# Optimization experiments

Measured on AMD Instinct MI355X. Metric: run time of the kernel, lower is better.

Reference implementation:

```python
import jax, jax.numpy as jnp
import numpy as np

D, H, L, V, BS = 1024, 16, 12, 50257, 2048
HD = D // H
EPS = 1e-5


def _ln(x, w, b):
    m = jnp.mean(x, -1, keepdims=True)
    v = jnp.mean(jnp.square(x - m), -1, keepdims=True)
    return (x - m) * jax.lax.rsqrt(v + EPS) * w + b


def setup_inputs() -> dict:
    key = jax.random.key(0)
    ks = jax.random.split(key, 10)
    B, T = 4, 1024
    s = 0.02
    return {
        "idx": jax.random.randint(ks[0], (B, T), 0, V),
        "targets": jax.random.randint(ks[1], (B, T), 0, V),
        "wte": s * jax.random.normal(ks[2], (V, D), jnp.float32),
        "wpe": s * jax.random.normal(ks[3], (BS, D), jnp.float32),
        "ln1_w": jnp.ones((L, D), jnp.float32),
        "ln1_b": jnp.zeros((L, D), jnp.float32),
        "qkv_w": s * jax.random.normal(ks[4], (L, D, 3 * D), jnp.float32),
        "qkv_b": jnp.zeros((L, 3 * D), jnp.float32),
        "o_w": s * jax.random.normal(ks[5], (L, D, D), jnp.float32),
        "o_b": jnp.zeros((L, D), jnp.float32),
        "ln2_w": jnp.ones((L, D), jnp.float32),
        "ln2_b": jnp.zeros((L, D), jnp.float32),
        "up_w": s * jax.random.normal(ks[6], (L, D, 4 * D), jnp.float32),
        "up_b": jnp.zeros((L, 4 * D), jnp.float32),
        "down_w": s * jax.random.normal(ks[7], (L, 4 * D, D), jnp.float32),
        "down_b": jnp.zeros((L, D), jnp.float32),
        "lnf_w": jnp.ones((D,), jnp.float32),
        "lnf_b": jnp.zeros((D,), jnp.float32),
        "lm_b": jnp.zeros((V,), jnp.float32),
    }


def _gpt(idx, targets, wte, wpe, ln1_w, ln1_b, qkv_w, qkv_b, o_w, o_b,
         ln2_w, ln2_b, up_w, up_b, down_w, down_b, lnf_w, lnf_b, lm_b):
    B, T = idx.shape
    x = wte[idx] + wpe[:T][None, :, :]  # [B,T,D]
    causal = jnp.tril(jnp.ones((T, T), bool))
    scale = HD ** -0.5

    def block(h, p):
        (l1w, l1b, qw, qb, ow, ob, l2w, l2b, uw, ub, dw, db) = p
        y = _ln(h, l1w, l1b)
        qkv = y @ qw + qb  # [B,T,3D]
        q, k, v = jnp.split(qkv, 3, axis=-1)
        q = q.reshape(B, T, H, HD)
        k = k.reshape(B, T, H, HD)
        v = v.reshape(B, T, H, HD)
        scores = jnp.einsum('bqhd,bkhd->bhqk', q, k) * scale
        scores = jnp.where(causal, scores, -jnp.inf)
        attn = jax.nn.softmax(scores, axis=-1)
        o = jnp.einsum('bhqk,bkhd->bqhd', attn, v).reshape(B, T, D)
        h = h + o @ ow + ob
        y = _ln(h, l2w, l2b)
        y = jax.nn.gelu(y @ uw + ub, approximate=False)
        h = h + y @ dw + db
        return h, None

    params = (ln1_w, ln1_b, qkv_w, qkv_b, o_w, o_b, ln2_w, ln2_b, up_w, up_b, down_w, down_b)
    x, _ = jax.lax.scan(block, x, params)
    x = _ln(x, lnf_w, lnf_b)
    logits = x @ wte.T + lm_b  # tied lm_head weight
    logp = jax.nn.log_softmax(logits, axis=-1)
    nll = -jnp.take_along_axis(logp, targets[..., None], axis=-1)[..., 0]
    loss = jnp.mean(nll)
    return logits, loss


def reference(idx, targets, wte, wpe, ln1_w, ln1_b, qkv_w, qkv_b, o_w, o_b,
              ln2_w, ln2_b, up_w, up_b, down_w, down_b, lnf_w, lnf_b, lm_b):
    return _gpt(idx, targets, wte, wpe, ln1_w, ln1_b, qkv_w, qkv_b, o_w, o_b,
                ln2_w, ln2_b, up_w, up_b, down_w, down_b, lnf_w, lnf_b, lm_b)
```

## Files before the change

kernel.cpp:

```cpp
#include <hip/hip_runtime.h>
#include <hip/hip_bf16.h>
#include <math.h>

typedef __attribute__((ext_vector_type(8))) short bfrag;
typedef __attribute__((ext_vector_type(4))) float f32x4;

static constexpr int Dm = 1024, Hh = 16, HD = 64, Ll = 12, Tt = 1024, Bb = 4;
static constexpr int Vv = 50257, Mrows = 4096;

__device__ inline unsigned short f2bf(float f) {
    unsigned u = __float_as_uint(f);
    u += 0x7fffu + ((u >> 16) & 1u);
    return (unsigned short)(u >> 16);
}
__device__ inline float bf2f(unsigned short s) {
    return __uint_as_float(((unsigned)s) << 16);
}

__device__ inline void gload16(const unsigned short* g, unsigned short* l) {
    __builtin_amdgcn_global_load_lds(
        (const __attribute__((address_space(1))) void*)g,
        (__attribute__((address_space(3))) void*)l, 16, 0, 0);
}

__global__ __launch_bounds__(256)
void embed_kernel(float* __restrict__ x, const float* __restrict__ wte,
                  const float* __restrict__ wpe, const int* __restrict__ idx) {
    int row = blockIdx.x;
    int t = row & (Tt - 1);
    int id = idx[row];
    int c = threadIdx.x * 4;
    float4 a = *reinterpret_cast<const float4*>(&wte[(size_t)id * Dm + c]);
    float4 p = *reinterpret_cast<const float4*>(&wpe[(size_t)t * Dm + c]);
    float4 o;
    o.x = a.x + p.x; o.y = a.y + p.y; o.z = a.z + p.z; o.w = a.w + p.w;
    *reinterpret_cast<float4*>(&x[(size_t)row * Dm + c]) = o;
}

__global__ __launch_bounds__(256)
void ln_kernel(unsigned short* __restrict__ y, const float* __restrict__ x,
               const float* __restrict__ w, const float* __restrict__ b) {
    int row = blockIdx.x;
    int tid = threadIdx.x;
    int lane = tid & 63, wv = tid >> 6;
    const float* xr = x + (size_t)row * Dm;
    float4 v = *reinterpret_cast<const float4*>(&xr[tid * 4]);
    float s1 = v.x + v.y + v.z + v.w;
    float s2 = v.x * v.x + v.y * v.y + v.z * v.z + v.w * v.w;
#pragma unroll
    for (int off = 1; off < 64; off <<= 1) {
        s1 += __shfl_xor(s1, off);
        s2 += __shfl_xor(s2, off);
    }
    __shared__ float r1[4], r2[4];
    if (lane == 0) { r1[wv] = s1; r2[wv] = s2; }
    __syncthreads();
    s1 = r1[0] + r1[1] + r1[2] + r1[3];
    s2 = r2[0] + r2[1] + r2[2] + r2[3];
    float mean = s1 * (1.0f / Dm);
    float var = s2 * (1.0f / Dm) - mean * mean;
    float rstd = rsqrtf(var + 1e-5f);
    float4 wvv = *reinterpret_cast<const float4*>(&w[tid * 4]);
    float4 bv = *reinterpret_cast<const float4*>(&b[tid * 4]);
    ushort4 o;
    o.x = f2bf((v.x - mean) * rstd * wvv.x + bv.x);
    o.y = f2bf((v.y - mean) * rstd * wvv.y + bv.y);
    o.z = f2bf((v.z - mean) * rstd * wvv.z + bv.z);
    o.w = f2bf((v.w - mean) * rstd * wvv.w + bv.w);
    *reinterpret_cast<ushort4*>(&y[(size_t)row * Dm + tid * 4]) = o;
}

__global__ __launch_bounds__(256)
void transpose_layer(const float* __restrict__ qw, const float* __restrict__ ow,
                     const float* __restrict__ uw, const float* __restrict__ dw,
                     unsigned short* __restrict__ wTq, unsigned short* __restrict__ wTo,
                     unsigned short* __restrict__ wTu, unsigned short* __restrict__ wTd) {
    __shared__ float t[32][33];
    int tb = blockIdx.x;
    const float* src; unsigned short* dst; int K, N, nx, base;
    if (tb < 3072)      { src = qw; dst = wTq; K = 1024; N = 3072; nx = 96;  base = 0; }
    else if (tb < 4096) { src = ow; dst = wTo; K = 1024; N = 1024; nx = 32;  base = 3072; }
    else if (tb < 8192) { src = uw; dst = wTu; K = 1024; N = 4096; nx = 128; base = 4096; }
    else                { src = dw; dst = wTd; K = 4096; N = 1024; nx = 32;  base = 8192; }
    int tt = tb - base;
    int n0 = (tt % nx) * 32, k0 = (tt / nx) * 32;
    int tid = threadIdx.x;
    int r = tid >> 3, c4 = (tid & 7) * 4;
    float4 v = *reinterpret_cast<const float4*>(&src[(size_t)(k0 + r) * N + n0 + c4]);
    t[r][c4] = v.x; t[r][c4 + 1] = v.y; t[r][c4 + 2] = v.z; t[r][c4 + 3] = v.w;
    __syncthreads();
    int nr = tid >> 3, kc = (tid & 7) * 4;
    ushort4 o;
    o.x = f2bf(t[kc][nr]);
    o.y = f2bf(t[kc + 1][nr]);
    o.z = f2bf(t[kc + 2][nr]);
    o.w = f2bf(t[kc + 3][nr]);
    *reinterpret_cast<ushort4*>(&dst[(size_t)(n0 + nr) * K + k0 + kc]) = o;
}

__global__ __launch_bounds__(128)
void cvt_rows(unsigned short* __restrict__ dst, const float* __restrict__ src) {
    int row = blockIdx.x;
    int t = threadIdx.x;
    const float* s = src + (size_t)row * Dm + t * 8;
    float4 f0 = *reinterpret_cast<const float4*>(s);
    float4 f1 = *reinterpret_cast<const float4*>(s + 4);
    ushort4 o0, o1;
    o0.x = f2bf(f0.x); o0.y = f2bf(f0.y); o0.z = f2bf(f0.z); o0.w = f2bf(f0.w);
    o1.x = f2bf(f1.x); o1.y = f2bf(f1.y); o1.z = f2bf(f1.z); o1.w = f2bf(f1.w);
    unsigned short* d = dst + (size_t)row * Dm + t * 8;
    *reinterpret_cast<ushort4*>(d) = o0;
    *reinterpret_cast<ushort4*>(d + 4) = o1;
}

template<int EPI, int GN>
__global__ __launch_bounds__(512, 2)
void gemm256(const unsigned short* __restrict__ A, const unsigned short* __restrict__ B,
             const float* __restrict__ bias, void* __restrict__ Cp,
             int Nv, int K, int ldc, int ncol) {
    __shared__ unsigned short As[4][256 * 32];
    __shared__ unsigned short Bs[4][256 * 32];
    const int tid = threadIdx.x;
    const int lane = tid & 63, w = tid >> 6;
    const int wr = w >> 2, wc = w & 3;
    const int g = lane >> 4, lr = lane & 15;
    const int slotk = (lr >> 1) & 3;

    const int gx = gridDim.x;
    int flat = blockIdx.y * gx + blockIdx.x;
    int nwg = gx * gridDim.y;
    {
        int q = nwg >> 3, rr = nwg & 7;
        int xcd = flat & 7, pos = flat >> 3;
        flat = ((xcd < rr) ? (xcd * (q + 1)) : (rr * (q + 1) + (xcd - rr) * q)) + pos;
    }
    const int bm = (flat % gx) * 256;
    const int bn = (flat / gx) * 256;

    const int srow = lane >> 2;
    const int gsrc = (lane & 3) ^ ((lane >> 3) & 3);
    const int rA0 = (w * 2 + 0) * 16 + srow;
    const int rA1 = (w * 2 + 1) * 16 + srow;
    const size_t aoff0 = (size_t)(bm + rA0) * K + gsrc * 8;
    const size_t aoff1 = (size_t)(bm + rA1) * K + gsrc * 8;
    int gb0 = bn + rA0, gb1 = bn + rA1;
    if (GN) { gb0 = (gb0 < Nv) ? gb0 : (Nv - 1); gb1 = (gb1 < Nv) ? gb1 : (Nv - 1); }
    const size_t boff0 = (size_t)gb0 * K + gsrc * 8;
    const size_t boff1 = (size_t)gb1 * K + gsrc * 8;
    unsigned short* lA0 = &As[0][(w * 2 + 0) * 512];
    unsigned short* lA1 = &As[0][(w * 2 + 1) * 512];
    unsigned short* lB0 = &Bs[0][(w * 2 + 0) * 512];
    unsigned short* lB1 = &Bs[0][(w * 2 + 1) * 512];

    const int nt = K >> 5;

    f32x4 acc[8][4];
#pragma unroll
    for (int i = 0; i < 8; ++i)
#pragma unroll
        for (int j = 0; j < 4; ++j)
#pragma unroll
            for (int r = 0; r < 4; ++r) acc[i][j][r] = 0.f;

#pragma unroll
    for (int tp = 0; tp < 3; ++tp) {
        const int kp = tp << 5;
        gload16(A + aoff0 + kp, lA0 + tp * 8192);
        gload16(B + boff0 + kp, lB0 + tp * 8192);
        gload16(A + aoff1 + kp, lA1 + tp * 8192);
        gload16(B + boff1 + kp, lB1 + tp * 8192);
    }
    asm volatile("s_waitcnt vmcnt(8)" ::: "memory");
    asm volatile("s_barrier" ::: "memory");

    for (int t = 0; t < nt; ++t) {
        const int bt = t & 3;
        const unsigned short* as = As[bt];
        const unsigned short* bs = Bs[bt];
        const int pf = t + 3;
        const int kp = pf << 5;
        const int so = (pf & 3) * 8192;

        bfrag bfr[4], af[8];
#pragma unroll
        for (int ni = 0; ni < 4; ++ni) {
            int row = wc * 64 + ni * 16 + lr;
            bfr[ni] = *reinterpret_cast<const bfrag*>(&bs[row * 32 + ((g ^ slotk) * 8)]);
        }
#pragma unroll
        for (int mi = 0; mi < 8; ++mi) {
            int row = wr * 128 + mi * 16 + lr;
            af[mi] = *reinterpret_cast<const bfrag*>(&as[row * 32 + ((g ^ slotk) * 8)]);
        }
        if (pf < nt) {
            gload16(A + aoff0 + kp, lA0 + so);
            gload16(B + boff0 + kp, lB0 + so);
            gload16(A + aoff1 + kp, lA1 + so);
            gload16(B + boff1 + kp, lB1 + so);
        }
        __builtin_amdgcn_s_setprio(1);
#pragma unroll
        for (int mi = 0; mi < 8; ++mi)
#pragma unroll
            for (int ni = 0; ni < 4; ++ni)
                acc[mi][ni] = __builtin_amdgcn_mfma_f32_16x16x32_bf16(
                    af[mi], bfr[ni], acc[mi][ni], 0, 0, 0);
        __builtin_amdgcn_s_setprio(0);
        if (t + 3 < nt)      asm volatile("s_waitcnt vmcnt(8)" ::: "memory");
        else if (t + 2 < nt) asm volatile("s_waitcnt vmcnt(4)" ::: "memory");
        else if (t + 1 < nt) asm volatile("s_waitcnt vmcnt(0)" ::: "memory");
        asm volatile("s_barrier" ::: "memory");
    }

    unsigned short* Cb = (unsigned short*)Cp;
    float* Cf = (float*)Cp;
#pragma unroll
    for (int ni = 0; ni < 4; ++ni) {
        int col = bn + wc * 64 + ni * 16 + lr;
        if (GN && col >= Nv) continue;
        int gcol = ncol + col;
        float bi = bias[gcol];
#pragma unroll
        for (int mi = 0; mi < 8; ++mi) {
            int row0 = bm + wr * 128 + mi * 16 + g * 4;
#pragma unroll
            for (int r = 0; r < 4; ++r) {
                int row = row0 + r;
                float v = acc[mi][ni][r] + bi;
                if (EPI == 0) {
                    Cb[(size_t)row * ldc + gcol] = f2bf(v);
                } else if (EPI == 1) {
                    v = 0.5f * v * (1.0f + erff(v * 0.70710678118654752f));
                    Cb[(size_t)row * ldc + gcol] = f2bf(v);
                } else {
                    Cf[(size_t)row * ldc + gcol] = v;
                }
            }
        }
    }
}

template<int EPI>
__global__ __launch_bounds__(256, 2)
void gemm128p(const unsigned short* __restrict__ A, const unsigned short* __restrict__ B,
              const float* __restrict__ bias, const float* __restrict__ R,
              void* __restrict__ Cp, int K, int ldc) {
    __shared__ unsigned short As[4][128 * 32];
    __shared__ unsigned short Bs[4][128 * 32];
    const int tid = threadIdx.x;
    const int lane = tid & 63, w = tid >> 6;
    const int wr = w >> 1, wc = w & 1;
    const int g = lane >> 4, lr = lane & 15;
    const int slotk = (lr >> 1) & 3;

    const int gx = gridDim.x;
    int flat = blockIdx.y * gx + blockIdx.x;
    int nwg = gx * gridDim.y;
    {
        int q = nwg >> 3, rr = nwg & 7;
        int xcd = flat & 7, pos = flat >> 3;
        flat = ((xcd < rr) ? (xcd * (q + 1)) : (rr * (q + 1) + (xcd - rr) * q)) + pos;
    }
    const int bm = (flat % gx) * 128;
    const int bn = (flat / gx) * 128;

    const int srow = lane >> 2;
    const int gsrc = (lane & 3) ^ ((lane >> 3) & 3);
    const int rA0 = (w * 2 + 0) * 16 + srow;
    const int rA1 = (w * 2 + 1) * 16 + srow;
    const size_t aoff0 = (size_t)(bm + rA0) * K + gsrc * 8;
    const size_t aoff1 = (size_t)(bm + rA1) * K + gsrc * 8;
    const size_t boff0 = (size_t)(bn + rA0) * K + gsrc * 8;
    const size_t boff1 = (size_t)(bn + rA1) * K + gsrc * 8;
    unsigned short* lA0 = &As[0][(w * 2 + 0) * 512];
    unsigned short* lA1 = &As[0][(w * 2 + 1) * 512];
    unsigned short* lB0 = &Bs[0][(w * 2 + 0) * 512];
    unsigned short* lB1 = &Bs[0][(w * 2 + 1) * 512];

    const int nt = K >> 5;

    f32x4 acc[4][4];
#pragma unroll
    for (int i = 0; i < 4; ++i)
#pragma unroll
        for (int j = 0; j < 4; ++j)
#pragma unroll
            for (int r = 0; r < 4; ++r) acc[i][j][r] = 0.f;

#pragma unroll
    for (int tp = 0; tp < 3; ++tp) {
        const int kp = tp << 5;
        gload16(A + aoff0 + kp, lA0 + tp * 4096);
        gload16(B + boff0 + kp, lB0 + tp * 4096);
        gload16(A + aoff1 + kp, lA1 + tp * 4096);
        gload16(B + boff1 + kp, lB1 + tp * 4096);
    }
    asm volatile("s_waitcnt vmcnt(8)" ::: "memory");
    asm volatile("s_barrier" ::: "memory");

    for (int t = 0; t < nt; ++t) {
        const int bt = t & 3;
        const unsigned short* as = As[bt];
        const unsigned short* bs = Bs[bt];
        const int pf = t + 3;
        const int kp = pf << 5;
        const int so = (pf & 3) * 4096;

        bfrag af[4], bfr[4];
#pragma unroll
        for (int i = 0; i < 4; ++i) {
            int ra = wr * 64 + i * 16 + lr;
            af[i] = *reinterpret_cast<const bfrag*>(&as[ra * 32 + ((g ^ slotk) * 8)]);
            int rb = wc * 64 + i * 16 + lr;
            bfr[i] = *reinterpret_cast<const bfrag*>(&bs[rb * 32 + ((g ^ slotk) * 8)]);
        }
        if (pf < nt) {
            gload16(A + aoff0 + kp, lA0 + so);
            gload16(B + boff0 + kp, lB0 + so);
            gload16(A + aoff1 + kp, lA1 + so);
            gload16(B + boff1 + kp, lB1 + so);
        }
        __builtin_amdgcn_s_setprio(1);
#pragma unroll
        for (int mi = 0; mi < 4; ++mi)
#pragma unroll
            for (int ni = 0; ni < 4; ++ni)
                acc[mi][ni] = __builtin_amdgcn_mfma_f32_16x16x32_bf16(
                    af[mi], bfr[ni], acc[mi][ni], 0, 0, 0);
        __builtin_amdgcn_s_setprio(0);
        if (t + 3 < nt)      asm volatile("s_waitcnt vmcnt(8)" ::: "memory");
        else if (t + 2 < nt) asm volatile("s_waitcnt vmcnt(4)" ::: "memory");
        else if (t + 1 < nt) asm volatile("s_waitcnt vmcnt(0)" ::: "memory");
        asm volatile("s_barrier" ::: "memory");
    }

    unsigned short* Cb = (unsigned short*)Cp;
    float* Cf = (float*)Cp;
#pragma unroll
    for (int ni = 0; ni < 4; ++ni) {
        int col = bn + wc * 64 + ni * 16 + lr;
        float bi = bias[col];
#pragma unroll
        for (int mi = 0; mi < 4; ++mi) {
            int row0 = bm + wr * 64 + mi * 16 + g * 4;
#pragma unroll
            for (int r = 0; r < 4; ++r) {
                int row = row0 + r;
                float v = acc[mi][ni][r] + bi;
                if (EPI == 0) {
                    Cb[(size_t)row * ldc + col] = f2bf(v);
                } else {
                    Cf[(size_t)row * ldc + col] = R[(size_t)row * ldc + col] + v;
                }
            }
        }
    }
}

__global__ __launch_bounds__(256)
void attn_mfma(const unsigned short* __restrict__ qkv, unsigned short* __restrict__ ob) {
    const int bq = blockIdx.x;
    const int h = blockIdx.y;
    const int b = blockIdx.z;
    const int tid = threadIdx.x, lane = tid & 63, w = tid >> 6;
    const int g = lane >> 4, lr = lane & 15;
    const int qg0 = bq * 128 + w * 32;

    __shared__ unsigned short Kt[64 * 72];
    __shared__ unsigned short Vt[64 * 72];
    __shared__ unsigned short Pl[4][32 * 72];
    unsigned short* Plw = Pl[w];

    bfrag aq[2][2];
#pragma unroll
    for (int qs = 0; qs < 2; ++qs)
#pragma unroll
        for (int ks = 0; ks < 2; ++ks) {
            int row = qg0 + qs * 16 + lr;
            aq[qs][ks] = *reinterpret_cast<const bfrag*>(
                &qkv[(size_t)(b * Tt + row) * 3072 + h * 64 + ks * 32 + g * 8]);
        }

    float mrow[2][4], lrow[2][4], osc[2][4];
    f32x4 oacc[2][4];
#pragma unroll
    for (int qs = 0; qs < 2; ++qs)
#pragma unroll
        for (int r = 0; r < 4; ++r) { mrow[qs][r] = -3.0e38f; lrow[qs][r] = 0.f; }
#pragma unroll
    for (int qs = 0; qs < 2; ++qs)
#pragma unroll
        for (int dn = 0; dn < 4; ++dn)
#pragma unroll
            for (int r = 0; r < 4; ++r) oacc[qs][dn][r] = 0.f;

    const int ntile = 2 * bq + 2;
    for (int kt = 0; kt < ntile; ++kt) {
        {
            int row = tid >> 2, seg = tid & 3;
            const unsigned short* sk =
                &qkv[(size_t)(b * Tt + kt * 64 + row) * 3072 + Dm + h * 64 + seg * 16];
            bfrag kv0 = *(const bfrag*)sk;
            bfrag kv1 = *(const bfrag*)(sk + 8);
            *reinterpret_cast<bfrag*>(&Kt[row * 72 + seg * 16]) = kv0;
            *reinterpret_cast<bfrag*>(&Kt[row * 72 + seg * 16 + 8]) = kv1;
            const uint4* sv = reinterpret_cast<const uint4*>(
                &qkv[(size_t)(b * Tt + kt * 64 + row) * 3072 + 2 * Dm + h * 64 + seg * 16]);
            uint4 u0 = sv[0], u1 = sv[1];
            uint4 a, r0, r1;
            a.x = (seg & 1) ? u0.y : u0.x; a.y = (seg & 1) ? u0.z : u0.y;
            a.z = (seg & 1) ? u0.w : u0.z; a.w = (seg & 1) ? u0.x : u0.w;
            r0.x = (seg & 2) ? a.z : a.x; r0.y = (seg & 2) ? a.w : a.y;
            r0.z = (seg & 2) ? a.x : a.z; r0.w = (seg & 2) ? a.y : a.w;
            a.x = (seg & 1) ? u1.y : u1.x; a.y = (seg & 1) ? u1.z : u1.y;
            a.z = (seg & 1) ? u1.w : u1.z; a.w = (seg & 1) ? u1.x : u1.w;
            r1.x = (seg & 2) ? a.z : a.x; r1.y = (seg & 2) ? a.w : a.y;
            r1.z = (seg & 2) ? a.x : a.z; r1.w = (seg & 2) ? a.y : a.w;
            unsigned w0[4] = {r0.x, r0.y, r0.z, r0.w};
            unsigned w1[4] = {r1.x, r1.y, r1.z, r1.w};
#pragma unroll
            for (int i = 0; i < 8; ++i) {
                int j = (i + 2 * seg) & 7;
                unsigned ww = w0[i >> 1];
                unsigned short val = (i & 1) ? (unsigned short)(ww >> 16)
                                             : (unsigned short)(ww & 0xffff);
                Vt[(seg * 16 + j) * 72 + row] = val;
            }
#pragma unroll
            for (int i = 0; i < 8; ++i) {
                int j = (i + 2 * seg) & 7;
                unsigned ww = w1[i >> 1];
                unsigned short val = (i & 1) ? (unsigned short)(ww >> 16)
                                             : (unsigned short)(ww & 0xffff);
                Vt[(seg * 16 + 8 + j) * 72 + row] = val;
            }
        }
        __syncthreads();

        bool active = (kt * 64 <= qg0 + 31);
        if (active) {
            f32x4 s[2][4];
#pragma unroll
            for (int qs = 0; qs < 2; ++qs)
#pragma unroll
                for (int n = 0; n < 4; ++n)
#pragma unroll
                    for (int r = 0; r < 4; ++r) s[qs][n][r] = 0.f;
            bfrag bk[4][2];
#pragma unroll
            for (int n = 0; n < 4; ++n)
#pragma unroll
                for (int ks = 0; ks < 2; ++ks)
                    bk[n][ks] = *reinterpret_cast<const bfrag*>(
                        &Kt[(n * 16 + lr) * 72 + ks * 32 + g * 8]);
#pragma unroll
            for (int qs = 0; qs < 2; ++qs)
#pragma unroll
                for (int n = 0; n < 4; ++n)
#pragma unroll
                    for (int ks = 0; ks < 2; ++ks)
                        s[qs][n] = __builtin_amdgcn_mfma_f32_16x16x32_bf16(
                            aq[qs][ks], bk[n][ks], s[qs][n], 0, 0, 0);

            bool mayMask = (kt * 64 + 63 > qg0);
            float pv[2][4][4];
#pragma unroll
            for (int qs = 0; qs < 2; ++qs) {
#pragma unroll
                for (int r = 0; r < 4; ++r) {
                    int qrow = qg0 + qs * 16 + g * 4 + r;
                    float v[4];
#pragma unroll
                    for (int n = 0; n < 4; ++n) {
                        float sv = s[qs][n][r] * 0.125f;
                        if (mayMask && (kt * 64 + n * 16 + lr > qrow)) sv = -3.0e38f;
                        v[n] = sv;
                    }
                    float tmax = fmaxf(fmaxf(v[0], v[1]), fmaxf(v[2], v[3]));
                    tmax = fmaxf(tmax, __shfl_xor(tmax, 1));
                    tmax = fmaxf(tmax, __shfl_xor(tmax, 2));
                    tmax = fmaxf(tmax, __shfl_xor(tmax, 4));
                    tmax = fmaxf(tmax, __shfl_xor(tmax, 8));
                    float mold = mrow[qs][r];
                    float mnew = fmaxf(mold, tmax);
                    float scl = expf(mold - mnew);
                    float psum = 0.f;
#pragma unroll
                    for (int n = 0; n < 4; ++n) {
                        float p = expf(v[n] - mnew);
                        pv[qs][n][r] = p;
                        psum += p;
                    }
                    psum += __shfl_xor(psum, 1);
                    psum += __shfl_xor(psum, 2);
                    psum += __shfl_xor(psum, 4);
                    psum += __shfl_xor(psum, 8);
                    lrow[qs][r] = lrow[qs][r] * scl + psum;
                    mrow[qs][r] = mnew;
                    osc[qs][r] = scl;
                }
            }
#pragma unroll
            for (int qs = 0; qs < 2; ++qs)
#pragma unroll
                for (int dn = 0; dn < 4; ++dn)
#pragma unroll
                    for (int r = 0; r < 4; ++r) oacc[qs][dn][r] *= osc[qs][r];
#pragma unroll
            for (int qs = 0; qs < 2; ++qs)
#pragma unroll
                for (int n = 0; n < 4; ++n)
#pragma unroll
                    for (int r = 0; r < 4; ++r)
                        Plw[(qs * 16 + g * 4 + r) * 72 + n * 16 + lr] = f2bf(pv[qs][n][r]);
            asm volatile("s_waitcnt lgkmcnt(0)" ::: "memory");
            bfrag ap[2][2], bv[4][2];
#pragma unroll
            for (int qs = 0; qs < 2; ++qs)
#pragma unroll
                for (int ks = 0; ks < 2; ++ks)
                    ap[qs][ks] = *reinterpret_cast<const bfrag*>(
                        &Plw[(qs * 16 + lr) * 72 + ks * 32 + g * 8]);
#pragma unroll
            for (int dn = 0; dn < 4; ++dn)
#pragma unroll
                for (int ks = 0; ks < 2; ++ks)
                    bv[dn][ks] = *reinterpret_cast<const bfrag*>(
                        &Vt[(dn * 16 + lr) * 72 + ks * 32 + g * 8]);
#pragma unroll
            for (int qs = 0; qs < 2; ++qs)
#pragma unroll
                for (int dn = 0; dn < 4; ++dn)
#pragma unroll
                    for (int ks = 0; ks < 2; ++ks)
                        oacc[qs][dn] = __builtin_amdgcn_mfma_f32_16x16x32_bf16(
                            ap[qs][ks], bv[dn][ks], oacc[qs][dn], 0, 0, 0);
        }
        __syncthreads();
    }

#pragma unroll
    for (int qs = 0; qs < 2; ++qs)
#pragma unroll
        for (int r = 0; r < 4; ++r) {
            float rinv = 1.0f / lrow[qs][r];
            int qrow = qg0 + qs * 16 + g * 4 + r;
#pragma unroll
            for (int dn = 0; dn < 4; ++dn)
                ob[(size_t)(b * Tt + qrow) * Dm + h * 64 + dn * 16 + lr] =
                    f2bf(oacc[qs][dn][r] * rinv);
        }
}

__global__ __launch_bounds__(512)
void loss_row_kernel(float* __restrict__ nll, const float* __restrict__ logits,
                     const int* __restrict__ targets) {
    const int row = blockIdx.x;
    const int tid = threadIdx.x;
    const int lane = tid & 63, wv = tid >> 6;
    const float* lr = logits + (size_t)row * Vv;

    const int lead = (4 - (row & 3)) & 3;
    const int nvec = (Vv - lead) >> 2;
    const int tail = Vv - lead - (nvec << 2);

    float m = -3.0e38f, s = 0.f;
    if (tid < lead) {
        float v = lr[tid];
        m = v; s = 1.f;
    }
    for (int k = tid; k < nvec; k += 512) {
        float4 v = *reinterpret_cast<const float4*>(lr + lead + (k << 2));
        float tm = fmaxf(fmaxf(v.x, v.y), fmaxf(v.z, v.w));
        float nm = fmaxf(m, tm);
        s = s * __expf(m - nm)
          + __expf(v.x - nm) + __expf(v.y - nm) + __expf(v.z - nm) + __expf(v.w - nm);
        m = nm;
    }
    if (tid < tail) {
        float v = lr[lead + (nvec << 2) + tid];
        float nm = fmaxf(m, v);
        s = s * __expf(m - nm) + __expf(v - nm);
        m = nm;
    }
#pragma unroll
    for (int off = 1; off < 64; off <<= 1) {
        float om = __shfl_xor(m, off);
        float os = __shfl_xor(s, off);
        float nm = fmaxf(m, om);
        s = s * __expf(m - nm) + os * __expf(om - nm);
        m = nm;
    }
    __shared__ float rm[8], rs[8];
    if (lane == 0) { rm[wv] = m; rs[wv] = s; }
    __syncthreads();
    if (tid == 0) {
        float M = rm[0];
#pragma unroll
        for (int i = 1; i < 8; ++i) M = fmaxf(M, rm[i]);
        float S = 0.f;
#pragma unroll
        for (int i = 0; i < 8; ++i) S += rs[i] * __expf(rm[i] - M);
        float lse = M + __logf(S);
        nll[row] = lse - lr[targets[row]];
    }
}

__global__ __launch_bounds__(256)
void loss_reduce_kernel(float* __restrict__ loss, const float* __restrict__ nll) {
    int tid = threadIdx.x;
    __shared__ float red[256];
    float s = 0.f;
    for (int j = tid; j < Mrows; j += 256) s += nll[j];
    red[tid] = s;
    __syncthreads();
    for (int st = 128; st > 0; st >>= 1) {
        if (tid < st) red[tid] += red[tid + st];
        __syncthreads();
    }
    if (tid == 0) *loss = red[0] * (1.0f / Mrows);
}

extern "C" void kernel_launch(void* const* d_in, const int* in_sizes, int n_in,
                              void* d_out, int out_size, void* d_ws, size_t ws_size,
                              hipStream_t stream) {
    const int* idx = (const int*)d_in[0];
    const int* targets = (const int*)d_in[1];
    const float* wte = (const float*)d_in[2];
    const float* wpe = (const float*)d_in[3];
    const float* ln1_w = (const float*)d_in[4];
    const float* ln1_b = (const float*)d_in[5];
    const float* qkv_w = (const float*)d_in[6];
    const float* qkv_b = (const float*)d_in[7];
    const float* o_w = (const float*)d_in[8];
    const float* o_b = (const float*)d_in[9];
    const float* ln2_w = (const float*)d_in[10];
    const float* ln2_b = (const float*)d_in[11];
    const float* up_w = (const float*)d_in[12];
    const float* up_b = (const float*)d_in[13];
    const float* down_w = (const float*)d_in[14];
    const float* down_b = (const float*)d_in[15];
    const float* lnf_w = (const float*)d_in[16];
    const float* lnf_b = (const float*)d_in[17];
    const float* lm_b = (const float*)d_in[18];

    float* logits = (float*)d_out;
    char* ws = (char*)d_ws;
    const size_t MB = 1 << 20;
    float* x            = (float*)(ws);
    unsigned short* y   = (unsigned short*)(ws + 16 * MB);
    unsigned short* qkv = (unsigned short*)(ws + 24 * MB);
    unsigned short* ob  = (unsigned short*)(ws + 48 * MB);
    unsigned short* up  = (unsigned short*)(ws + 56 * MB);
    unsigned short* wTq = (unsigned short*)(ws + 88 * MB);
    unsigned short* wTo = (unsigned short*)(ws + 96 * MB);
    unsigned short* wTu = (unsigned short*)(ws + 100 * MB);
    unsigned short* wTd = (unsigned short*)(ws + 112 * MB);
    float* nll          = (float*)(ws + 127 * MB);
    unsigned short* wbf = (unsigned short*)(ws + 24 * MB);

    embed_kernel<<<Mrows, 256, 0, stream>>>(x, wte, wpe, idx);

    for (int l = 0; l < Ll; ++l) {
        ln_kernel<<<Mrows, 256, 0, stream>>>(y, x, ln1_w + l * Dm, ln1_b + l * Dm);
        transpose_layer<<<12288, 256, 0, stream>>>(
            qkv_w + (size_t)l * Dm * 3 * Dm, o_w + (size_t)l * Dm * Dm,
            up_w + (size_t)l * Dm * 4 * Dm, down_w + (size_t)l * 4 * Dm * Dm,
            wTq, wTo, wTu, wTd);
        gemm128p<0><<<dim3(Mrows / 128, 3 * Dm / 128), 256, 0, stream>>>(
            y, wTq, qkv_b + (size_t)l * 3 * Dm, nullptr, qkv, Dm, 3 * Dm);
        attn_mfma<<<dim3(8, Hh, Bb), 256, 0, stream>>>(qkv, ob);
        gemm128p<2><<<dim3(Mrows / 128, Dm / 128), 256, 0, stream>>>(
            ob, wTo, o_b + (size_t)l * Dm, x, x, Dm, Dm);
        ln_kernel<<<Mrows, 256, 0, stream>>>(y, x, ln2_w + l * Dm, ln2_b + l * Dm);
        gemm256<1, 0><<<dim3(Mrows / 256, 4 * Dm / 256), 512, 0, stream>>>(
            y, wTu, up_b + (size_t)l * 4 * Dm, up, 4 * Dm, Dm, 4 * Dm, 0);
        gemm128p<2><<<dim3(Mrows / 128, Dm / 128), 256, 0, stream>>>(
            up, wTd, down_b + (size_t)l * Dm, x, x, 4 * Dm, Dm);
    }

    ln_kernel<<<Mrows, 256, 0, stream>>>(y, x, lnf_w, lnf_b);

    cvt_rows<<<Vv, 128, 0, stream>>>(wbf, wte);
    gemm256<3, 1><<<dim3(Mrows / 256, (Vv + 255) / 256), 512, 0, stream>>>(
        y, wbf, lm_b, logits, Vv, Dm, Vv, 0);

    loss_row_kernel<<<Mrows, 512, 0, stream>>>(nll, logits, targets);
    loss_reduce_kernel<<<1, 256, 0, stream>>>(logits + (size_t)Mrows * Vv, nll);
}
```

Measured before the change: 4.622 ms.

## Switch gemm256 to double-buffered BK=64 tiles with nontemporal fp32 stores

Restructures the 256x256 GEMM mainloop from a 4-stage ring of K=32 tiles to a 2-stage double buffer of K=64 tiles. Each thread now loads 16B rows with an 8-way XOR swizzle, and each loaded tile feeds two MFMA sub-steps. This halves the number of barriers and waitcnts per K and lowers occupancy to 1 block per CU, which lets the compiler use more registers. In exchange only one tile is prefetched ahead, so global-load latency is less well hidden. The fp32 epilogue, used for the large logits output, now writes with nontemporal stores to reduce cache pollution.

```diff
diff --git a/kernel.cpp b/kernel.cpp
--- a/kernel.cpp
+++ b/kernel.cpp
@@ -114,17 +114,16 @@
 }
 
 template<int EPI, int GN>
-__global__ __launch_bounds__(512, 2)
+__global__ __launch_bounds__(512, 1)
 void gemm256(const unsigned short* __restrict__ A, const unsigned short* __restrict__ B,
              const float* __restrict__ bias, void* __restrict__ Cp,
              int Nv, int K, int ldc, int ncol) {
-    __shared__ unsigned short As[4][256 * 32];
-    __shared__ unsigned short Bs[4][256 * 32];
+    __shared__ unsigned short As[2][256 * 64];
+    __shared__ unsigned short Bs[2][256 * 64];
     const int tid = threadIdx.x;
     const int lane = tid & 63, w = tid >> 6;
     const int wr = w >> 2, wc = w & 3;
     const int g = lane >> 4, lr = lane & 15;
-    const int slotk = (lr >> 1) & 3;
 
     const int gx = gridDim.x;
     int flat = blockIdx.y * gx + blockIdx.x;
@@ -137,22 +136,19 @@
     const int bm = (flat % gx) * 256;
     const int bn = (flat / gx) * 256;
 
-    const int srow = lane >> 2;
-    const int gsrc = (lane & 3) ^ ((lane >> 3) & 3);
-    const int rA0 = (w * 2 + 0) * 16 + srow;
-    const int rA1 = (w * 2 + 1) * 16 + srow;
-    const size_t aoff0 = (size_t)(bm + rA0) * K + gsrc * 8;
-    const size_t aoff1 = (size_t)(bm + rA1) * K + gsrc * 8;
-    int gb0 = bn + rA0, gb1 = bn + rA1;
-    if (GN) { gb0 = (gb0 < Nv) ? gb0 : (Nv - 1); gb1 = (gb1 < Nv) ? gb1 : (Nv - 1); }
-    const size_t boff0 = (size_t)gb0 * K + gsrc * 8;
-    const size_t boff1 = (size_t)gb1 * K + gsrc * 8;
-    unsigned short* lA0 = &As[0][(w * 2 + 0) * 512];
-    unsigned short* lA1 = &As[0][(w * 2 + 1) * 512];
-    unsigned short* lB0 = &Bs[0][(w * 2 + 0) * 512];
-    unsigned short* lB1 = &Bs[0][(w * 2 + 1) * 512];
-
-    const int nt = K >> 5;
+    const int srow = tid >> 3;
+    const int gsrc = (tid & 7) ^ (srow & 7);
+    size_t aoff[4], boff[4];
+#pragma unroll
+    for (int j = 0; j < 4; ++j) {
+        int ra = bm + j * 64 + srow;
+        aoff[j] = (size_t)ra * K + gsrc * 8;
+        int rb = bn + j * 64 + srow;
+        if (GN) rb = (rb < Nv) ? rb : (Nv - 1);
+        boff[j] = (size_t)rb * K + gsrc * 8;
+    }
+
+    const int nt = K >> 6;
 
     f32x4 acc[8][4];
 #pragma unroll
@@ -163,53 +159,54 @@
             for (int r = 0; r < 4; ++r) acc[i][j][r] = 0.f;
 
 #pragma unroll
-    for (int tp = 0; tp < 3; ++tp) {
-        const int kp = tp << 5;
-        gload16(A + aoff0 + kp, lA0 + tp * 8192);
-        gload16(B + boff0 + kp, lB0 + tp * 8192);
-        gload16(A + aoff1 + kp, lA1 + tp * 8192);
-        gload16(B + boff1 + kp, lB1 + tp * 8192);
-    }
-    asm volatile("s_waitcnt vmcnt(8)" ::: "memory");
+    for (int j = 0; j < 4; ++j) {
+        gload16(A + aoff[j], &As[0][j * 4096 + tid * 8]);
+        gload16(B + boff[j], &Bs[0][j * 4096 + tid * 8]);
+    }
+    asm volatile("s_waitcnt vmcnt(0)" ::: "memory");
     asm volatile("s_barrier" ::: "memory");
 
     for (int t = 0; t < nt; ++t) {
-        const int bt = t & 3;
-        const unsigned short* as = As[bt];
-        const unsigned short* bs = Bs[bt];
-        const int pf = t + 3;
-        const int kp = pf << 5;
-        const int so = (pf & 3) * 8192;
-
-        bfrag bfr[4], af[8];
-#pragma unroll
-        for (int ni = 0; ni < 4; ++ni) {
-            int row = wc * 64 + ni * 16 + lr;
-            bfr[ni] = *reinterpret_cast<const bfrag*>(&bs[row * 32 + ((g ^ slotk) * 8)]);
-        }
-#pragma unroll
-        for (int mi = 0; mi < 8; ++mi) {
-            int row = wr * 128 + mi * 16 + lr;
-            af[mi] = *reinterpret_cast<const bfrag*>(&as[row * 32 + ((g ^ slotk) * 8)]);
-        }
-        if (pf < nt) {
-            gload16(A + aoff0 + kp, lA0 + so);
-            gload16(B + boff0 + kp, lB0 + so);
-            gload16(A + aoff1 + kp, lA1 + so);
-            gload16(B + boff1 + kp, lB1 + so);
-        }
-        __builtin_amdgcn_s_setprio(1);
-#pragma unroll
-        for (int mi = 0; mi < 8; ++mi)
-#pragma unroll
-            for (int ni = 0; ni < 4; ++ni)
-                acc[mi][ni] = __builtin_amdgcn_mfma_f32_16x16x32_bf16(
-                    af[mi], bfr[ni], acc[mi][ni], 0, 0, 0);
-        __builtin_amdgcn_s_setprio(0);
-        if (t + 3 < nt)      asm volatile("s_waitcnt vmcnt(8)" ::: "memory");
-        else if (t + 2 < nt) asm volatile("s_waitcnt vmcnt(4)" ::: "memory");
-        else if (t + 1 < nt) asm volatile("s_waitcnt vmcnt(0)" ::: "memory");
-        asm volatile("s_barrier" ::: "memory");
+        const int sl = t & 1;
+        const unsigned short* as = As[sl];
+        const unsigned short* bs = Bs[sl];
+        if (t + 1 < nt) {
+            const int so = (t + 1) & 1;
+            const size_t kp = (size_t)(t + 1) << 6;
+#pragma unroll
+            for (int j = 0; j < 4; ++j) {
+                gload16(A + aoff[j] + kp, &As[so][j * 4096 + tid * 8]);
+                gload16(B + boff[j] + kp, &Bs[so][j * 4096 + tid * 8]);
+            }
+        }
+#pragma unroll
+        for (int ks = 0; ks < 2; ++ks) {
+            bfrag bfr[4], af[8];
+#pragma unroll
+            for (int ni = 0; ni < 4; ++ni) {
+                int row = wc * 64 + ni * 16 + lr;
+                bfr[ni] = *reinterpret_cast<const bfrag*>(
+                    &bs[row * 64 + (((ks * 4 + g) ^ (row & 7)) * 8)]);
+            }
+#pragma unroll
+            for (int mi = 0; mi < 8; ++mi) {
+                int row = wr * 128 + mi * 16 + lr;
+                af[mi] = *reinterpret_cast<const bfrag*>(
+                    &as[row * 64 + (((ks * 4 + g) ^ (row & 7)) * 8)]);
+            }
+            __builtin_amdgcn_s_setprio(1);
+#pragma unroll
+            for (int mi = 0; mi < 8; ++mi)
+#pragma unroll
+                for (int ni = 0; ni < 4; ++ni)
+                    acc[mi][ni] = __builtin_amdgcn_mfma_f32_16x16x32_bf16(
+                        af[mi], bfr[ni], acc[mi][ni], 0, 0, 0);
+            __builtin_amdgcn_s_setprio(0);
+        }
+        if (t + 1 < nt) {
+            asm volatile("s_waitcnt vmcnt(0)" ::: "memory");
+            asm volatile("s_barrier" ::: "memory");
+        }
     }
 
     unsigned short* Cb = (unsigned short*)Cp;
@@ -233,7 +230,7 @@
                     v = 0.5f * v * (1.0f + erff(v * 0.70710678118654752f));
                     Cb[(size_t)row * ldc + gcol] = f2bf(v);
                 } else {
-                    Cf[(size_t)row * ldc + gcol] = v;
+                    __builtin_nontemporal_store(v, &Cf[(size_t)row * ldc + gcol]);
                 }
             }
         }
```

Measured after the change: 4.735 ms. 1.02x slower.

## Fuse softmax partial reductions into LM-head GEMM epilogue

Applied to the files above, without the earlier changes.

The LM-head GEMM epilogue now computes per-row max and sum-exp partials for each 256-column tile, reduces them within the block through LDS, and writes them to a small buffer. A lightweight combine kernel merges these partials per row to get the log-sum-exp and NLL. This removes the full second pass over the fp32 logits matrix. The trade-off is extra exp and shuffle work in the GEMM epilogue and an added LDS barrier, and logits are now written with nontemporal stores.

```diff
diff --git a/kernel.cpp b/kernel.cpp
--- a/kernel.cpp
+++ b/kernel.cpp
@@ -7,6 +7,7 @@
 
 static constexpr int Dm = 1024, Hh = 16, HD = 64, Ll = 12, Tt = 1024, Bb = 4;
 static constexpr int Vv = 50257, Mrows = 4096;
+static constexpr int PLD = 200;
 
 __device__ inline unsigned short f2bf(float f) {
     unsigned u = __float_as_uint(f);
@@ -117,7 +118,8 @@
 __global__ __launch_bounds__(512, 2)
 void gemm256(const unsigned short* __restrict__ A, const unsigned short* __restrict__ B,
              const float* __restrict__ bias, void* __restrict__ Cp,
-             int Nv, int K, int ldc, int ncol) {
+             int Nv, int K, int ldc, int ncol,
+             float* __restrict__ pm_out, float* __restrict__ ps_out) {
     __shared__ unsigned short As[4][256 * 32];
     __shared__ unsigned short Bs[4][256 * 32];
     const int tid = threadIdx.x;
@@ -214,28 +216,88 @@
 
     unsigned short* Cb = (unsigned short*)Cp;
     float* Cf = (float*)Cp;
-#pragma unroll
-    for (int ni = 0; ni < 4; ++ni) {
-        int col = bn + wc * 64 + ni * 16 + lr;
-        if (GN && col >= Nv) continue;
-        int gcol = ncol + col;
-        float bi = bias[gcol];
-#pragma unroll
-        for (int mi = 0; mi < 8; ++mi) {
-            int row0 = bm + wr * 128 + mi * 16 + g * 4;
-#pragma unroll
-            for (int r = 0; r < 4; ++r) {
-                int row = row0 + r;
-                float v = acc[mi][ni][r] + bi;
-                if (EPI == 0) {
-                    Cb[(size_t)row * ldc + gcol] = f2bf(v);
-                } else if (EPI == 1) {
-                    v = 0.5f * v * (1.0f + erff(v * 0.70710678118654752f));
-                    Cb[(size_t)row * ldc + gcol] = f2bf(v);
-                } else {
-                    Cf[(size_t)row * ldc + gcol] = v;
+
+    if (EPI != 4) {
+#pragma unroll
+        for (int ni = 0; ni < 4; ++ni) {
+            int col = bn + wc * 64 + ni * 16 + lr;
+            if (GN && col >= Nv) continue;
+            int gcol = ncol + col;
+            float bi = bias[gcol];
+#pragma unroll
+            for (int mi = 0; mi < 8; ++mi) {
+                int row0 = bm + wr * 128 + mi * 16 + g * 4;
+#pragma unroll
+                for (int r = 0; r < 4; ++r) {
+                    int row = row0 + r;
+                    float v = acc[mi][ni][r] + bi;
+                    if (EPI == 0) {
+                        Cb[(size_t)row * ldc + gcol] = f2bf(v);
+                    } else {
+                        v = 0.5f * v * (1.0f + erff(v * 0.70710678118654752f));
+                        Cb[(size_t)row * ldc + gcol] = f2bf(v);
+                    }
                 }
             }
+        }
+    } else {
+        __syncthreads();
+        float* lm = (float*)&As[0][0];
+        float* lsd = lm + 1024;
+        float bi4[4];
+        int colv[4];
+#pragma unroll
+        for (int ni = 0; ni < 4; ++ni) {
+            colv[ni] = bn + wc * 64 + ni * 16 + lr;
+            bi4[ni] = (colv[ni] < Nv) ? bias[ncol + colv[ni]] : 0.f;
+        }
+#pragma unroll
+        for (int mi = 0; mi < 8; ++mi) {
+#pragma unroll
+            for (int r = 0; r < 4; ++r) {
+                int row = bm + wr * 128 + mi * 16 + g * 4 + r;
+                float vv[4];
+                float ml = -3.0e38f, sl = 0.f;
+#pragma unroll
+                for (int ni = 0; ni < 4; ++ni) {
+                    float v = acc[mi][ni][r] + bi4[ni];
+                    vv[ni] = v;
+                    if (colv[ni] < Nv) ml = fmaxf(ml, v);
+                }
+#pragma unroll
+                for (int ni = 0; ni < 4; ++ni) {
+                    if (colv[ni] < Nv) {
+                        sl += __expf(vv[ni] - ml);
+                        __builtin_nontemporal_store(
+                            vv[ni], &Cf[(size_t)row * ldc + ncol + colv[ni]]);
+                    }
+                }
+#pragma unroll
+                for (int off = 1; off < 16; off <<= 1) {
+                    float om = __shfl_xor(ml, off);
+                    float os = __shfl_xor(sl, off);
+                    float nm = fmaxf(ml, om);
+                    sl = sl * __expf(ml - nm) + os * __expf(om - nm);
+                    ml = nm;
+                }
+                if (lr == 0) {
+                    int lrow = wr * 128 + mi * 16 + g * 4 + r;
+                    lm[lrow * 4 + wc] = ml;
+                    lsd[lrow * 4 + wc] = sl;
+                }
+            }
+        }
+        __syncthreads();
+        if (tid < 256) {
+            float m0 = lm[tid * 4 + 0], m1 = lm[tid * 4 + 1];
+            float m2 = lm[tid * 4 + 2], m3 = lm[tid * 4 + 3];
+            float M = fmaxf(fmaxf(m0, m1), fmaxf(m2, m3));
+            float S = lsd[tid * 4 + 0] * __expf(m0 - M) + lsd[tid * 4 + 1] * __expf(m1 - M)
+                    + lsd[tid * 4 + 2] * __expf(m2 - M) + lsd[tid * 4 + 3] * __expf(m3 - M);
+            int row = bm + tid;
+            int bno = bn >> 8;
+            pm_out[(size_t)row * PLD + bno] = M;
+            ps_out[(size_t)row * PLD + bno] = S;
         }
     }
 }
@@ -552,35 +614,18 @@
         }
 }
 
-__global__ __launch_bounds__(512)
-void loss_row_kernel(float* __restrict__ nll, const float* __restrict__ logits,
-                     const int* __restrict__ targets) {
+__global__ __launch_bounds__(64)
+void loss_combine(float* __restrict__ nll, const float* __restrict__ pm,
+                  const float* __restrict__ ps, const float* __restrict__ logits,
+                  const int* __restrict__ targets, int nby) {
     const int row = blockIdx.x;
-    const int tid = threadIdx.x;
-    const int lane = tid & 63, wv = tid >> 6;
-    const float* lr = logits + (size_t)row * Vv;
-
-    const int lead = (4 - (row & 3)) & 3;
-    const int nvec = (Vv - lead) >> 2;
-    const int tail = Vv - lead - (nvec << 2);
-
+    const int lane = threadIdx.x;
     float m = -3.0e38f, s = 0.f;
-    if (tid < lead) {
-        float v = lr[tid];
-        m = v; s = 1.f;
-    }
-    for (int k = tid; k < nvec; k += 512) {
-        float4 v = *reinterpret_cast<const float4*>(lr + lead + (k << 2));
-        float tm = fmaxf(fmaxf(v.x, v.y), fmaxf(v.z, v.w));
-        float nm = fmaxf(m, tm);
-        s = s * __expf(m - nm)
-          + __expf(v.x - nm) + __expf(v.y - nm) + __expf(v.z - nm) + __expf(v.w - nm);
-        m = nm;
-    }
-    if (tid < tail) {
-        float v = lr[lead + (nvec << 2) + tid];
-        float nm = fmaxf(m, v);
-        s = s * __expf(m - nm) + __expf(v - nm);
+    for (int j = lane; j < nby; j += 64) {
+        float om = pm[(size_t)row * PLD + j];
+        float os = ps[(size_t)row * PLD + j];
+        float nm = fmaxf(m, om);
+        s = s * __expf(m - nm) + os * __expf(om - nm);
         m = nm;
     }
 #pragma unroll
@@ -591,18 +636,9 @@
         s = s * __expf(m - nm) + os * __expf(om - nm);
         m = nm;
     }
-    __shared__ float rm[8], rs[8];
-    if (lane == 0) { rm[wv] = m; rs[wv] = s; }
-    __syncthreads();
-    if (tid == 0) {
-        float M = rm[0];
-#pragma unroll
-        for (int i = 1; i < 8; ++i) M = fmaxf(M, rm[i]);
-        float S = 0.f;
-#pragma unroll
-        for (int i = 0; i < 8; ++i) S += rs[i] * __expf(rm[i] - M);
-        float lse = M + __logf(S);
-        nll[row] = lse - lr[targets[row]];
+    if (lane == 0) {
+        float lse = m + __logf(s);
+        nll[row] = lse - logits[(size_t)row * Vv + targets[row]];
     }
 }
 
@@ -658,6 +694,8 @@
     unsigned short* wTd = (unsigned short*)(ws + 112 * MB);
     float* nll          = (float*)(ws + 127 * MB);
     unsigned short* wbf = (unsigned short*)(ws + 24 * MB);
+    float* pmp          = (float*)(ws + 131 * MB);
+    float* psp          = (float*)(ws + 136 * MB);
 
     embed_kernel<<<Mrows, 256, 0, stream>>>(x, wte, wpe, idx);
 
@@ -674,7 +712,8 @@
             ob, wTo, o_b + (size_t)l * Dm, x, x, Dm, Dm);
         ln_kernel<<<Mrows, 256, 0, stream>>>(y, x, ln2_w + l * Dm, ln2_b + l * Dm);
         gemm256<1, 0><<<dim3(Mrows / 256, 4 * Dm / 256), 512, 0, stream>>>(
-            y, wTu, up_b + (size_t)l * 4 * Dm, up, 4 * Dm, Dm, 4 * Dm, 0);
+            y, wTu, up_b + (size_t)l * 4 * Dm, up, 4 * Dm, Dm, 4 * Dm, 0,
+            nullptr, nullptr);
         gemm128p<2><<<dim3(Mrows / 128, Dm / 128), 256, 0, stream>>>(
             up, wTd, down_b + (size_t)l * Dm, x, x, 4 * Dm, Dm);
     }
@@ -682,9 +721,10 @@
     ln_kernel<<<Mrows, 256, 0, stream>>>(y, x, lnf_w, lnf_b);
 
     cvt_rows<<<Vv, 128, 0, stream>>>(wbf, wte);
-    gemm256<3, 1><<<dim3(Mrows / 256, (Vv + 255) / 256), 512, 0, stream>>>(
-        y, wbf, lm_b, logits, Vv, Dm, Vv, 0);
-
-    loss_row_kernel<<<Mrows, 512, 0, stream>>>(nll, logits, targets);
+    const int NBY = (Vv + 255) / 256;
+    gemm256<4, 1><<<dim3(Mrows / 256, NBY), 512, 0, stream>>>(
+        y, wbf, lm_b, logits, Vv, Dm, Vv, 0, pmp, psp);
+
+    loss_combine<<<Mrows, 64, 0, stream>>>(nll, pmp, psp, logits, targets, NBY);
     loss_reduce_kernel<<<1, 256, 0, stream>>>(logits + (size_t)Mrows * Vv, nll);
 }
```

Result: faster. 4.336 ms (-6.2%).
